# Optimization experiments

Measured on AMD Instinct MI355X. Metric: run time of the kernel, lower is better.

Reference implementation:

```python
import jax, jax.numpy as jnp
import numpy as np

DIM, HID, BATCH = 64, 512, 8192


def setup_inputs() -> dict:
    key = jax.random.key(0)
    ks = jax.random.split(key, 6)
    s1 = 1.0 / np.sqrt(DIM + 1)
    s2 = 1.0 / np.sqrt(HID)
    return {
        "t": jax.random.uniform(ks[0], (1,), dtype=jnp.float32),
        "x": jax.random.normal(ks[1], (BATCH, DIM), dtype=jnp.float32),
        "W1": jax.random.normal(ks[2], (DIM + 1, HID), dtype=jnp.float32) * s1,
        "b1": jnp.zeros((HID,), jnp.float32),
        "W2": jax.random.normal(ks[3], (HID, HID), dtype=jnp.float32) * s2,
        "b2": jnp.zeros((HID,), jnp.float32),
        "W3": jax.random.normal(ks[4], (HID, DIM), dtype=jnp.float32) * s2,
        "b3": jnp.zeros((DIM,), jnp.float32),
    }


def _vf_single(ts, xs, W1, b1, W2, b2, W3, b3):
    # xs: [dim], ts: scalar. Time concatenated as extra input feature.
    h = jnp.concatenate([xs, ts[None]])          # [dim+1]
    h = jnp.tanh(h @ W1 + b1)                    # [hid]
    h = jnp.tanh(h @ W2 + b2)                    # [hid]
    return h @ W3 + b3                           # [dim]


def reference(t, x, W1, b1, W2, b2, W3, b3):
    ts = t[0]
    vf = lambda xs: _vf_single(ts, xs, W1, b1, W2, b2, W3, b3)
    v = jax.vmap(vf)(x)                                   # [B, dim]
    # Exact divergence: trace of per-sample Jacobian dv/dx.
    # (Replaces the torch per-dim autograd.grad loop with one batched jacfwd.)
    J = jax.vmap(jax.jacfwd(vf))(x)                       # [B, dim, dim]
    div = jnp.trace(J, axis1=-2, axis2=-1)                # [B]
    return (v, -div[:, None])
```

## Files before the change

kernel.cpp:

```cpp
#include <hip/hip_runtime.h>

#define DIM 64
#define HID 512
#define BATCH 8192
#define MB 32
#define NTHR 1024

typedef __attribute__((ext_vector_type(8))) short short8;
typedef __attribute__((ext_vector_type(4))) float f32x4;
typedef __attribute__((ext_vector_type(16))) float f32x16;
typedef float float4_ __attribute__((ext_vector_type(4)));
typedef unsigned long long ull;

#define Z16 {0.f,0.f,0.f,0.f,0.f,0.f,0.f,0.f,0.f,0.f,0.f,0.f,0.f,0.f,0.f,0.f}

union U8 { short8 s8; unsigned short u[8]; };
union U4 { ull v; unsigned short u[4]; };
union FB { unsigned u; float f; };

__device__ __forceinline__ unsigned short f2bf(float f) {
    union { float f; unsigned u; } v; v.f = f;
    return (unsigned short)((v.u + 0x7FFFu + ((v.u >> 16) & 1u)) >> 16);
}
__device__ __forceinline__ float tanh_fast(float x) {
    float e = __expf(2.f * x);
    return 1.f - __fdividef(2.f, e + 1.f);
}

__global__ __launch_bounds__(256) void prep(
        const float* __restrict__ t,  const float* __restrict__ W1,
        const float* __restrict__ b1, const float* __restrict__ W2,
        const float* __restrict__ W3,
        unsigned short* __restrict__ w2pk, unsigned short* __restrict__ ppk,
        unsigned short* __restrict__ w3pk, unsigned short* __restrict__ w1pk,
        float* __restrict__ c1) {
    __shared__ float w3sT[DIM * 33];
    __shared__ float w1s[DIM * DIM];
    int b = blockIdx.x;
    if (b >= 288) {
        int n = (b - 288) * 256 + threadIdx.x;
        c1[n] = fmaf(t[0], W1[DIM * HID + n], b1[n]);
        return;
    }
    int gid = b * 256 + threadIdx.x;
    int f = gid >> 6, l = gid & 63;
    if (f < 512) {
        int nt = f >> 5, ks = f & 31;
        int n = nt * 32 + (l & 31), k0 = ks * 16 + (l >> 5) * 8;
        unsigned short* o = w2pk + (size_t)(f * 64 + l) * 8;
#pragma unroll
        for (int e = 0; e < 8; ++e) o[e] = f2bf(W2[(size_t)(k0 + e) * HID + n]);
    } else if (f < 1024) {
        int ntb = (b * 4 - 512) >> 5;
        int jb  = (((b - 128) * 4) & 31) * 16;
        for (int idx = threadIdx.x; idx < 32 * DIM; idx += 256) {
            int dn = idx >> 6, i = idx & 63;
            w3sT[i * 33 + dn] = W3[(size_t)(ntb * 32 + dn) * DIM + i];
        }
        for (int idx = threadIdx.x; idx < DIM * DIM; idx += 256) {
            int i = idx >> 6, jj = idx & 63;
            w1s[i * DIM + jj] = W1[(size_t)i * HID + jb + jj];
        }
        __syncthreads();
        int fi = f - 512;
        int ks = fi & 31;
        int dn = l & 31, k0 = ks * 16 + (l >> 5) * 8;
        int n = ntb * 32 + dn;
        int jo = k0 - jb;
        float m[8] = {0.f,0.f,0.f,0.f,0.f,0.f,0.f,0.f};
#pragma unroll
        for (int i = 0; i < DIM; ++i) {
            float w3 = w3sT[i * 33 + dn];
            const float* wrow = &w1s[i * DIM + jo];
#pragma unroll
            for (int e = 0; e < 8; ++e) m[e] = fmaf(wrow[e], w3, m[e]);
        }
        unsigned short* o = ppk + (size_t)(fi * 64 + l) * 8;
#pragma unroll
        for (int e = 0; e < 8; ++e) o[e] = f2bf(W2[(size_t)(k0 + e) * HID + n] * m[e]);
    } else if (f < 1088) {
        int fi = f - 1024;
        int nt = fi >> 4, ks = fi & 15;
        int n = nt * 16 + (l & 15), k0 = ks * 32 + (l >> 4) * 8;
        unsigned short* o = w3pk + (size_t)(fi * 64 + l) * 8;
#pragma unroll
        for (int e = 0; e < 8; ++e) o[e] = f2bf(W3[(size_t)(k0 + e) * DIM + n]);
    } else {
        int fi = f - 1088;
        int nt = fi >> 1, ks = fi & 1;
        int n = nt * 16 + (l & 15), k0 = ks * 32 + (l >> 4) * 8;
        unsigned short* o = w1pk + (size_t)(fi * 64 + l) * 8;
#pragma unroll
        for (int e = 0; e < 8; ++e) o[e] = f2bf(W1[(size_t)(k0 + e) * HID + n]);
    }
}

__device__ __forceinline__ int act_addr(int sample, int colbyte) {
    return (sample * 1024 + colbyte) ^ ((sample & 15) << 4);
}

__global__ __launch_bounds__(NTHR) void fused_main(
        const float* __restrict__ x,  const float* __restrict__ c1,
        const float* __restrict__ b2, const float* __restrict__ b3,
        const unsigned short* __restrict__ w1pk, const unsigned short* __restrict__ w2pk,
        const unsigned short* __restrict__ ppk,  const unsigned short* __restrict__ w3pk,
        float* __restrict__ out) {
    __shared__ unsigned short h1s[MB * HID];
    __shared__ unsigned short d1s[MB * HID];
    __shared__ unsigned short h2s[MB * HID];
    __shared__ float wred[16][MB];
    char* h1b = (char*)h1s; char* d1b = (char*)d1s; char* h2b = (char*)h2s;

    const int tid = threadIdx.x, w = tid >> 6, l = tid & 63;
    const int lr = l & 15, g = l >> 4;
    const int bid = blockIdx.x;
    const int s0 = bid * MB;

    short8 xf[2][2];
#pragma unroll
    for (int nt = 0; nt < 2; ++nt)
#pragma unroll
        for (int ks = 0; ks < 2; ++ks) {
            const float* xp = x + (size_t)(s0 + nt * 16 + lr) * DIM + ks * 32 + g * 8;
            float4_ x0 = *(const float4_*)xp;
            float4_ x1 = *(const float4_*)(xp + 4);
            U8 u;
            u.u[0]=f2bf(x0.x); u.u[1]=f2bf(x0.y); u.u[2]=f2bf(x0.z); u.u[3]=f2bf(x0.w);
            u.u[4]=f2bf(x1.x); u.u[5]=f2bf(x1.y); u.u[6]=f2bf(x1.z); u.u[7]=f2bf(x1.w);
            xf[nt][ks] = u.s8;
        }
#pragma unroll
    for (int mi = 0; mi < 2; ++mi) {
        int mt = w * 2 + mi;
        short8 a0 = ((const short8*)w1pk)[(size_t)((mt * 2 + 0) * 64 + l)];
        short8 a1 = ((const short8*)w1pk)[(size_t)((mt * 2 + 1) * 64 + l)];
        float c1q[4];
#pragma unroll
        for (int r = 0; r < 4; ++r) c1q[r] = c1[mt * 16 + g * 4 + r];
#pragma unroll
        for (int nt = 0; nt < 2; ++nt) {
            f32x4 acc = {0.f, 0.f, 0.f, 0.f};
            acc = __builtin_amdgcn_mfma_f32_16x16x32_bf16(a0, xf[nt][0], acc, 0, 0, 0);
            acc = __builtin_amdgcn_mfma_f32_16x16x32_bf16(a1, xf[nt][1], acc, 0, 0, 0);
            int sample = nt * 16 + lr;
            U4 hu, du;
#pragma unroll
            for (int r = 0; r < 4; ++r) {
                float h = tanh_fast(acc[r] + c1q[r]);
                hu.u[r] = f2bf(h);
                du.u[r] = f2bf(fmaf(-h, h, 1.f));
            }
            int ab = act_addr(sample, (mt * 16 + g * 4) * 2);
            *(ull*)(h1b + ab) = hu.v;
            *(ull*)(d1b + ab) = du.v;
        }
    }
    __syncthreads();

    const int q2 = (w + bid) & 15;
    const int rot = (bid * 5) & 31;
    const short8* bwp = (const short8*)w2pk + (size_t)(q2 * 32) * 64 + l;
    const short8* bpp = (const short8*)ppk  + (size_t)(q2 * 32) * 64 + l;

    f32x16 zacc = Z16;
#pragma unroll 4
    for (int i = 0; i < 32; ++i) {
        int ks = (i + rot) & 31;
        short8 av = *(const short8*)(h1b + act_addr(l & 31, ks * 32 + (l >> 5) * 16));
        zacc = __builtin_amdgcn_mfma_f32_32x32x16_bf16(av, bwp[ks * 64], zacc, 0, 0, 0);
    }
    f32x16 sacc = Z16;
#pragma unroll 4
    for (int i = 0; i < 32; ++i) {
        int ks = (i + rot) & 31;
        short8 ad = *(const short8*)(d1b + act_addr(l & 31, ks * 32 + (l >> 5) * 16));
        sacc = __builtin_amdgcn_mfma_f32_32x32x16_bf16(ad, bpp[ks * 64], sacc, 0, 0, 0);
    }

    float divp[16];
    {
        int c = q2 * 32 + (l & 31);
        float b2v = b2[c];
#pragma unroll
        for (int r = 0; r < 16; ++r) {
            int row = (r & 3) + 8 * (r >> 2) + 4 * (l >> 5);
            float h2 = tanh_fast(zacc[r] + b2v);
            *(unsigned short*)(h2b + act_addr(row, c * 2)) = f2bf(h2);
            divp[r] = sacc[r] * fmaf(-h2, h2, 1.f);
        }
    }
#pragma unroll
    for (int off = 1; off < 32; off <<= 1) {
#pragma unroll
        for (int r = 0; r < 16; ++r) divp[r] += __shfl_xor(divp[r], off, 64);
    }
    if ((l & 31) == 0) {
#pragma unroll
        for (int r = 0; r < 16; ++r) {
            int row = (r & 3) + 8 * (r >> 2) + 4 * (l >> 5);
            wred[w][row] = divp[r];
        }
    }
    __syncthreads();

    if (w < 8) {
        const int wm3 = w & 1, wn3 = w >> 1;
        const int rot3 = (bid * 3) & 15;
        f32x4 acc = {0.f, 0.f, 0.f, 0.f};
        const short8* W3f = (const short8*)w3pk + (size_t)(wn3 * 16) * 64 + l;
#pragma unroll
        for (int i = 0; i < 16; ++i) {
            int ks = (i + rot3) & 15;
            short8 ah = *(const short8*)(h2b + act_addr(wm3 * 16 + lr, ks * 64 + g * 16));
            acc = __builtin_amdgcn_mfma_f32_16x16x32_bf16(ah, W3f[ks * 64], acc, 0, 0, 0);
        }
        int c = wn3 * 16 + lr;
        float b3v = b3[c];
#pragma unroll
        for (int r = 0; r < 4; ++r)
            out[(size_t)(s0 + wm3 * 16 + g * 4 + r) * DIM + c] = acc[r] + b3v;
    }
    if (tid < MB) {
        float d = 0.f;
#pragma unroll
        for (int ww = 0; ww < 16; ++ww) d += wred[ww][tid];
        out[(size_t)BATCH * DIM + s0 + tid] = -d;
    }
}

extern "C" void kernel_launch(void* const* d_in, const int* in_sizes, int n_in,
                              void* d_out, int out_size, void* d_ws, size_t ws_size,
                              hipStream_t stream) {
    const float* t  = (const float*)d_in[0];
    const float* x  = (const float*)d_in[1];
    const float* W1 = (const float*)d_in[2];
    const float* b1 = (const float*)d_in[3];
    const float* W2 = (const float*)d_in[4];
    const float* b2 = (const float*)d_in[5];
    const float* W3 = (const float*)d_in[6];
    const float* b3 = (const float*)d_in[7];
    float* out = (float*)d_out;

    char* ws = (char*)d_ws;
    unsigned short* w2pk = (unsigned short*)ws;
    unsigned short* ppk  = (unsigned short*)(ws + (512 << 10));
    unsigned short* w3pk = (unsigned short*)(ws + (1 << 20));
    unsigned short* w1pk = (unsigned short*)(ws + (1 << 20) + (64 << 10));
    float*          c1   = (float*)(ws + (1 << 20) + (128 << 10));

    prep<<<290, 256, 0, stream>>>(t, W1, b1, W2, W3, w2pk, ppk, w3pk, w1pk, c1);
    fused_main<<<BATCH / MB, NTHR, 0, stream>>>(x, c1, b2, b3, w1pk, w2pk, ppk, w3pk, out);
}
```

Baseline: 32.86 us.

## Halve block threads, recompute tanh derivative from h1, drop d1 shared buffer

Blocks shrink from 1024 to 512 threads, so each wave now handles two layer-2 column tiles sequentially and accumulates its divergence partials across them. The d1 shared buffer (1-h1^2) is removed and recomputed on the fly from h1 in bf16 with a packed convert, cutting LDS use so more blocks fit per CU, with waves_per_eu pinned at 4. The per-block rotation of tile and k order, which spread global and LDS access, is also removed. The cost is extra VALU work in the inner loop and longer per-wave serial work.

Measured after the change: 42.55 us. 29.5% more time.

```diff
diff --git a/kernel.cpp b/kernel.cpp
--- a/kernel.cpp
+++ b/kernel.cpp
@@ -4,7 +4,7 @@
 #define HID 512
 #define BATCH 8192
 #define MB 32
-#define NTHR 1024
+#define NTHR 512
 
 typedef __attribute__((ext_vector_type(8))) short short8;
 typedef __attribute__((ext_vector_type(4))) float f32x4;
@@ -25,6 +25,21 @@
 __device__ __forceinline__ float tanh_fast(float x) {
     float e = __expf(2.f * x);
     return 1.f - __fdividef(2.f, e + 1.f);
+}
+__device__ __forceinline__ short8 d1_from_h1(short8 h) {
+    union { short8 s8; unsigned u[4]; } in, out;
+    in.s8 = h;
+#pragma unroll
+    for (int i = 0; i < 4; ++i) {
+        unsigned u = in.u[i];
+        FB lo, hi; lo.u = u << 16; hi.u = u & 0xffff0000u;
+        float dlo = fmaf(-lo.f, lo.f, 1.f);
+        float dhi = fmaf(-hi.f, hi.f, 1.f);
+        unsigned o;
+        asm("v_cvt_pk_bf16_f32 %0, %1, %2" : "=v"(o) : "v"(dlo), "v"(dhi));
+        out.u[i] = o;
+    }
+    return out.s8;
 }
 
 __global__ __launch_bounds__(256) void prep(
@@ -99,22 +114,22 @@
     return (sample * 1024 + colbyte) ^ ((sample & 15) << 4);
 }
 
-__global__ __launch_bounds__(NTHR) void fused_main(
+__global__ __launch_bounds__(NTHR)
+__attribute__((amdgpu_waves_per_eu(4, 4)))
+void fused_main(
         const float* __restrict__ x,  const float* __restrict__ c1,
         const float* __restrict__ b2, const float* __restrict__ b3,
         const unsigned short* __restrict__ w1pk, const unsigned short* __restrict__ w2pk,
         const unsigned short* __restrict__ ppk,  const unsigned short* __restrict__ w3pk,
         float* __restrict__ out) {
     __shared__ unsigned short h1s[MB * HID];
-    __shared__ unsigned short d1s[MB * HID];
     __shared__ unsigned short h2s[MB * HID];
-    __shared__ float wred[16][MB];
-    char* h1b = (char*)h1s; char* d1b = (char*)d1s; char* h2b = (char*)h2s;
+    __shared__ float wred[8][MB];
+    char* h1b = (char*)h1s; char* h2b = (char*)h2s;
 
     const int tid = threadIdx.x, w = tid >> 6, l = tid & 63;
     const int lr = l & 15, g = l >> 4;
-    const int bid = blockIdx.x;
-    const int s0 = bid * MB;
+    const int s0 = blockIdx.x * MB;
 
     short8 xf[2][2];
 #pragma unroll
@@ -130,8 +145,8 @@
             xf[nt][ks] = u.s8;
         }
 #pragma unroll
-    for (int mi = 0; mi < 2; ++mi) {
-        int mt = w * 2 + mi;
+    for (int mi = 0; mi < 4; ++mi) {
+        int mt = w * 4 + mi;
         short8 a0 = ((const short8*)w1pk)[(size_t)((mt * 2 + 0) * 64 + l)];
         short8 a1 = ((const short8*)w1pk)[(size_t)((mt * 2 + 1) * 64 + l)];
         float c1q[4];
@@ -143,74 +158,66 @@
             acc = __builtin_amdgcn_mfma_f32_16x16x32_bf16(a0, xf[nt][0], acc, 0, 0, 0);
             acc = __builtin_amdgcn_mfma_f32_16x16x32_bf16(a1, xf[nt][1], acc, 0, 0, 0);
             int sample = nt * 16 + lr;
-            U4 hu, du;
-#pragma unroll
-            for (int r = 0; r < 4; ++r) {
-                float h = tanh_fast(acc[r] + c1q[r]);
-                hu.u[r] = f2bf(h);
-                du.u[r] = f2bf(fmaf(-h, h, 1.f));
+            U4 hu;
+#pragma unroll
+            for (int r = 0; r < 4; ++r) hu.u[r] = f2bf(tanh_fast(acc[r] + c1q[r]));
+            *(ull*)(h1b + act_addr(sample, (mt * 16 + g * 4) * 2)) = hu.v;
+        }
+    }
+    __syncthreads();
+
+#pragma unroll 1
+    for (int j = 0; j < 2; ++j) {
+        const int nt = w * 2 + j;
+        const short8* bwp = (const short8*)w2pk + (size_t)(nt * 32) * 64 + l;
+        const short8* bpp = (const short8*)ppk  + (size_t)(nt * 32) * 64 + l;
+        f32x16 zacc = Z16;
+#pragma unroll 2
+        for (int ks = 0; ks < 32; ++ks) {
+            short8 av = *(const short8*)(h1b + act_addr(l & 31, ks * 32 + (l >> 5) * 16));
+            zacc = __builtin_amdgcn_mfma_f32_32x32x16_bf16(av, bwp[ks * 64], zacc, 0, 0, 0);
+        }
+        f32x16 sacc = Z16;
+#pragma unroll 2
+        for (int ks = 0; ks < 32; ++ks) {
+            short8 ah = *(const short8*)(h1b + act_addr(l & 31, ks * 32 + (l >> 5) * 16));
+            short8 ad = d1_from_h1(ah);
+            sacc = __builtin_amdgcn_mfma_f32_32x32x16_bf16(ad, bpp[ks * 64], sacc, 0, 0, 0);
+        }
+        float dp[16];
+        {
+            int c = nt * 32 + (l & 31);
+            float b2v = b2[c];
+#pragma unroll
+            for (int r = 0; r < 16; ++r) {
+                int row = (r & 3) + 8 * (r >> 2) + 4 * (l >> 5);
+                float h2 = tanh_fast(zacc[r] + b2v);
+                *(unsigned short*)(h2b + act_addr(row, c * 2)) = f2bf(h2);
+                dp[r] = sacc[r] * fmaf(-h2, h2, 1.f);
             }
-            int ab = act_addr(sample, (mt * 16 + g * 4) * 2);
-            *(ull*)(h1b + ab) = hu.v;
-            *(ull*)(d1b + ab) = du.v;
+        }
+#pragma unroll
+        for (int off = 1; off < 32; off <<= 1) {
+#pragma unroll
+            for (int r = 0; r < 16; ++r) dp[r] += __shfl_xor(dp[r], off, 64);
+        }
+        if ((l & 31) == 0) {
+#pragma unroll
+            for (int r = 0; r < 16; ++r) {
+                int row = (r & 3) + 8 * (r >> 2) + 4 * (l >> 5);
+                if (j == 0) wred[w][row] = dp[r];
+                else        wred[w][row] += dp[r];
+            }
         }
     }
     __syncthreads();
 
-    const int q2 = (w + bid) & 15;
-    const int rot = (bid * 5) & 31;
-    const short8* bwp = (const short8*)w2pk + (size_t)(q2 * 32) * 64 + l;
-    const short8* bpp = (const short8*)ppk  + (size_t)(q2 * 32) * 64 + l;
-
-    f32x16 zacc = Z16;
-#pragma unroll 4
-    for (int i = 0; i < 32; ++i) {
-        int ks = (i + rot) & 31;
-        short8 av = *(const short8*)(h1b + act_addr(l & 31, ks * 32 + (l >> 5) * 16));
-        zacc = __builtin_amdgcn_mfma_f32_32x32x16_bf16(av, bwp[ks * 64], zacc, 0, 0, 0);
-    }
-    f32x16 sacc = Z16;
-#pragma unroll 4
-    for (int i = 0; i < 32; ++i) {
-        int ks = (i + rot) & 31;
-        short8 ad = *(const short8*)(d1b + act_addr(l & 31, ks * 32 + (l >> 5) * 16));
-        sacc = __builtin_amdgcn_mfma_f32_32x32x16_bf16(ad, bpp[ks * 64], sacc, 0, 0, 0);
-    }
-
-    float divp[16];
     {
-        int c = q2 * 32 + (l & 31);
-        float b2v = b2[c];
-#pragma unroll
-        for (int r = 0; r < 16; ++r) {
-            int row = (r & 3) + 8 * (r >> 2) + 4 * (l >> 5);
-            float h2 = tanh_fast(zacc[r] + b2v);
-            *(unsigned short*)(h2b + act_addr(row, c * 2)) = f2bf(h2);
-            divp[r] = sacc[r] * fmaf(-h2, h2, 1.f);
-        }
-    }
-#pragma unroll
-    for (int off = 1; off < 32; off <<= 1) {
-#pragma unroll
-        for (int r = 0; r < 16; ++r) divp[r] += __shfl_xor(divp[r], off, 64);
-    }
-    if ((l & 31) == 0) {
-#pragma unroll
-        for (int r = 0; r < 16; ++r) {
-            int row = (r & 3) + 8 * (r >> 2) + 4 * (l >> 5);
-            wred[w][row] = divp[r];
-        }
-    }
-    __syncthreads();
-
-    if (w < 8) {
-        const int wm3 = w & 1, wn3 = w >> 1;
-        const int rot3 = (bid * 3) & 15;
+        const int wm3 = w >> 2, wn3 = w & 3;
         f32x4 acc = {0.f, 0.f, 0.f, 0.f};
         const short8* W3f = (const short8*)w3pk + (size_t)(wn3 * 16) * 64 + l;
 #pragma unroll
-        for (int i = 0; i < 16; ++i) {
-            int ks = (i + rot3) & 15;
+        for (int ks = 0; ks < 16; ++ks) {
             short8 ah = *(const short8*)(h2b + act_addr(wm3 * 16 + lr, ks * 64 + g * 16));
             acc = __builtin_amdgcn_mfma_f32_16x16x32_bf16(ah, W3f[ks * 64], acc, 0, 0, 0);
         }
@@ -223,7 +230,7 @@
     if (tid < MB) {
         float d = 0.f;
 #pragma unroll
-        for (int ww = 0; ww < 16; ++ww) d += wred[ww][tid];
+        for (int ww = 0; ww < 8; ++ww) d += wred[ww][tid];
         out[(size_t)BATCH * DIM + s0 + tid] = -d;
     }
 }
```
